# Performance work log

Hardware: AMD Instinct MI355X
Metric: run time of the kernel (lower is better)

## Reference

```python
import jax, jax.numpy as jnp
import numpy as np

LEAKY_SLOPE = 0.2
EPS = 1e-9


def setup_inputs() -> dict:
    key = jax.random.key(0)
    k1, k2, k3, k4 = jax.random.split(key, 4)
    B, N, F_in, F_out = 4, 4096, 128, 64
    h = jax.random.normal(k1, (B, N, F_in), dtype=jnp.float32)
    adj = jax.random.uniform(k2, (B, N, N), dtype=jnp.float32)
    W = jax.random.normal(k3, (F_in, F_out), dtype=jnp.float32) * (1.0 / np.sqrt(F_in))
    a = jax.random.normal(k4, (2 * F_out, 1), dtype=jnp.float32) * (1.0 / np.sqrt(2 * F_out))
    return {"h": h, "adj": adj, "W": W, "a": a}


def reference(h, adj, W, a):
    # h: [B,N,F_in], adj: [B,N,N], W: [F_in,F_out], a: [2F_out,1]
    Wh = jnp.einsum('bnf,fo->bno', h, W)  # [B,N,F_out]
    F_out = W.shape[1]
    a1 = a[:F_out, 0]   # applied to Wh1 (neighbor j features)
    a2 = a[F_out:, 0]   # applied to Wh2 (center i features)
    s1 = Wh @ a1        # [B,N] -> broadcast over j axis
    s2 = Wh @ a2        # [B,N] -> broadcast over i axis
    # e[b,i,j] = leaky_relu(Wh[b,j]@a1 + Wh[b,i]@a2)  (concat([Wh1,Wh2]) @ a)
    e = jax.nn.leaky_relu(s2[:, :, None] + s1[:, None, :], negative_slope=LEAKY_SLOPE)
    attn = jax.nn.softmax(e, axis=-1)          # dense softmax over all nodes
    attn = attn * adj                          # mask with adjacency
    attn = attn / (jnp.sum(attn, axis=-1, keepdims=True) + EPS)  # renormalize
    return jnp.einsum('bij,bjo->bio', attn, Wh)  # [B,N,F_out]
```

## Files before the change

### kernel.cpp

```cpp
#include <hip/hip_runtime.h>
#include <hip/hip_bf16.h>


typedef __attribute__((ext_vector_type(8))) short bf16x8;
typedef __attribute__((ext_vector_type(4))) float f32x4;
typedef __attribute__((ext_vector_type(4))) unsigned int u32x4;

#define LOG2E 1.4426950408889634f

__device__ __forceinline__ unsigned int pk2(float lo, float hi) {
  float2 f2; f2.x = lo; f2.y = hi;
  union { __hip_bfloat162 b; unsigned int u; } c;
  c.b = __float22bfloat162_rn(f2);
  return c.u;
}
__device__ __forceinline__ bf16x8 u2b(u32x4 v) {
  union { u32x4 u; bf16x8 b; } c; c.u = v; return c.b;
}
__device__ __forceinline__ float vexp2_(float x) {
  float r; asm("v_exp_f32 %0, %1" : "=v"(r) : "v"(x)); return r;
}

__global__ __launch_bounds__(256) void k_wh(
    const float* __restrict__ h, const float* __restrict__ W, const float* __restrict__ a,
    unsigned short* __restrict__ wt, float* __restrict__ s1, float* __restrict__ s2) {
  __shared__ float hs[32][130];
  __shared__ float Ws[128 * 64];
  const int t = threadIdx.x;
  const int b = blockIdx.x >> 7;
  const int row0 = (blockIdx.x & 127) << 5;

  #pragma unroll
  for (int it = 0; it < 8; ++it) {
    const int fidx = it * 256 + t;
    ((float4*)Ws)[fidx] = ((const float4*)W)[fidx];
  }
  #pragma unroll
  for (int it = 0; it < 4; ++it) {
    int flat = it * 256 + t;
    int r = flat >> 5, q = flat & 31;
    const float4 v = *(const float4*)(h + ((size_t)(b * 4096 + row0 + r)) * 128 + 4 * q);
    hs[r][4*q+0] = v.x; hs[r][4*q+1] = v.y; hs[r][4*q+2] = v.z; hs[r][4*q+3] = v.w;
  }
  __syncthreads();

  const int rg = t >> 4, cg = t & 15;
  float acc[2][4] = {};
  for (int k = 0; k < 128; ++k) {
    float4 wv = ((const float4*)Ws)[k * 16 + cg];
    #pragma unroll
    for (int i = 0; i < 2; ++i) {
      float hv = hs[2*rg + i][k];
      acc[i][0] = fmaf(hv, wv.x, acc[i][0]);
      acc[i][1] = fmaf(hv, wv.y, acc[i][1]);
      acc[i][2] = fmaf(hv, wv.z, acc[i][2]);
      acc[i][3] = fmaf(hv, wv.w, acc[i][3]);
    }
  }
  __syncthreads();

  float (*WhF)[68] = (float(*)[68])hs;
  #pragma unroll
  for (int i = 0; i < 2; ++i)
    #pragma unroll
    for (int j = 0; j < 4; ++j)
      WhF[2*rg + i][4*cg + j] = acc[i][j];
  __syncthreads();

  if (t < 32) {
    float x1 = 0.f, x2 = 0.f;
    #pragma unroll 8
    for (int c = 0; c < 64; ++c) {
      float v = WhF[t][c];
      x1 = fmaf(v, a[c], x1);
      x2 = fmaf(v, a[64 + c], x2);
    }
    s1[b * 4096 + row0 + t] = x1 * LOG2E;
    s2[b * 4096 + row0 + t] = x2 * LOG2E;
  }

  const int col = t >> 2, sub = t & 3;
  unsigned int uh[4];
  #pragma unroll
  for (int r = 0; r < 4; ++r)
    uh[r] = pk2(WhF[8*sub + 2*r][col], WhF[8*sub + 2*r + 1][col]);
  const int S = (b * 128 + (row0 >> 5)) * 4 + (col >> 4);
  unsigned short* dst = wt + ((size_t)S << 9) + sub * 128 + (col & 15) * 8;
  *(uint4*)dst = make_uint4(uh[0], uh[1], uh[2], uh[3]);
}

__global__ __launch_bounds__(256, 2) void k_main(
    const float* __restrict__ adj, const unsigned short* __restrict__ wt,
    const float* __restrict__ s1, const float* __restrict__ s2,
    float* __restrict__ out) {
  __shared__ unsigned short Pws[2][8192];
  __shared__ float Ss[32];

  const int t = threadIdx.x;
  const int blk = blockIdx.x;
  const int xcd = blk & 7;
  const int b = xcd >> 1;
  const int tile = (blk >> 3) + ((xcd & 1) << 6);
  const int row0 = tile << 5;
  const int l = t & 63, w = t >> 6;
  const int lr = l & 15, g = l >> 4;

  const float* adjW = adj + ((size_t)(b * 4096 + row0 + 8 * w)) * 4096 + 4 * l;
  const float* s1W  = s1 + b * 4096 + 4 * l;
  const unsigned short* wtW = wt + (((size_t)(b * 128) * 4 + w) << 9) + 8 * l;

  float s2r[8];
  #pragma unroll
  for (int r = 0; r < 8; ++r) s2r[r] = s2[b * 4096 + row0 + 8 * w + r];

  float sar[8] = {0.f,0.f,0.f,0.f,0.f,0.f,0.f,0.f};
  f32x4 acc0 = {0.f,0.f,0.f,0.f}, acc1 = {0.f,0.f,0.f,0.f};

  f32x4 aX[8], aY[8], sX, sY;
  u32x4 bv[8];

#define LOADADJ(av, sv, ks) do {                                              \
    const int ko = ((ks) & 15) << 8;                                          \
    _Pragma("unroll")                                                         \
    for (int r = 0; r < 8; ++r)                                               \
      av[r] = *(const f32x4*)(adjW + (size_t)r * 4096 + ko);                  \
    sv = *(const f32x4*)(s1W + ko);                                           \
  } while (0)

#define LOADB(ks) do {                                                        \
    const int ksm = (ks) & 15;                                                \
    const unsigned short* bp = wtW + ((size_t)(ksm * 8) << 11);               \
    _Pragma("unroll")                                                         \
    for (int kk = 0; kk < 8; ++kk)                                            \
      bv[kk] = *(const u32x4*)(bp + (kk << 11));                              \
  } while (0)

#define PBUILD(av, sv, buf) do {                                              \
    unsigned short* Pd = &Pws[buf][0];                                        \
    _Pragma("unroll")                                                         \
    for (int r = 0; r < 8; ++r) {                                             \
      float e0 = s2r[r] + sv[0], e1 = s2r[r] + sv[1];                         \
      float e2 = s2r[r] + sv[2], e3 = s2r[r] + sv[3];                         \
      e0 = fmaxf(e0, 0.2f * e0); e1 = fmaxf(e1, 0.2f * e1);                   \
      e2 = fmaxf(e2, 0.2f * e2); e3 = fmaxf(e3, 0.2f * e3);                   \
      float p0 = vexp2_(e0), p1 = vexp2_(e1);                                 \
      float p2 = vexp2_(e2), p3 = vexp2_(e3);                                 \
      float w0 = av[r][0] * p0, w1 = av[r][1] * p1;                           \
      float w2 = av[r][2] * p2, w3 = av[r][3] * p3;                           \
      sar[r] += (w0 + w1) + (w2 + w3);                                        \
      uint2 pk; pk.x = pk2(w0, w1); pk.y = pk2(w2, w3);                       \
      *(uint2*)(Pd + (8 * w + r) * 256 + ((4 * l) ^ (r << 3))) = pk;          \
    }                                                                         \
  } while (0)

#define SYNC() do {                                                           \
    asm volatile("s_waitcnt lgkmcnt(0)" ::: "memory");                        \
    __builtin_amdgcn_sched_barrier(0);                                        \
    __builtin_amdgcn_s_barrier();                                             \
    __builtin_amdgcn_sched_barrier(0);                                        \
  } while (0)

#define MFMAP(buf) do {                                                       \
    const unsigned short* Pr = &Pws[buf][0];                                  \
    _Pragma("unroll")                                                         \
    for (int kk = 0; kk < 8; ++kk) {                                          \
      const int koff = (8 * g + 32 * kk) ^ ((lr & 7) << 3);                   \
      bf16x8 a0 = *(const bf16x8*)(Pr + lr * 256 + koff);                     \
      bf16x8 a1 = *(const bf16x8*)(Pr + (16 + lr) * 256 + koff);              \
      acc0 = __builtin_amdgcn_mfma_f32_16x16x32_bf16(a0, u2b(bv[kk]), acc0, 0, 0, 0); \
      acc1 = __builtin_amdgcn_mfma_f32_16x16x32_bf16(a1, u2b(bv[kk]), acc1, 0, 0, 0); \
    }                                                                         \
  } while (0)

  LOADADJ(aX, sX, 0);
  LOADADJ(aY, sY, 1);
  LOADB(0);

  for (int it = 0; it < 8; ++it) {
    PBUILD(aX, sX, 0);
    LOADADJ(aX, sX, 2 * it + 2);
    SYNC();
    MFMAP(0);
    LOADB(2 * it + 1);

    PBUILD(aY, sY, 1);
    LOADADJ(aY, sY, 2 * it + 3);
    SYNC();
    MFMAP(1);
    LOADB(2 * it + 2);
  }

  #pragma unroll
  for (int r = 0; r < 8; ++r) {
    float v = sar[r];
    #pragma unroll
    for (int m = 1; m < 64; m <<= 1) v += __shfl_xor(v, m);
    sar[r] = v;
  }
  if (l == 0) {
    #pragma unroll
    for (int r = 0; r < 8; ++r) Ss[8 * w + r] = sar[r];
  }
  __syncthreads();

  #pragma unroll
  for (int reg = 0; reg < 4; ++reg) {
    const int r0 = 4 * g + reg, r1 = 16 + 4 * g + reg;
    const float i0 = 1.0f / Ss[r0], i1 = 1.0f / Ss[r1];
    const size_t ob = ((size_t)(b * 4096 + row0 + r0)) * 64 + 16 * w + lr;
    out[ob] = acc0[reg] * i0;
    out[ob + (size_t)16 * 64] = acc1[reg] * i1;
  }
}

extern "C" void kernel_launch(void* const* d_in, const int* in_sizes, int n_in,
                              void* d_out, int out_size, void* d_ws, size_t ws_size,
                              hipStream_t stream) {
  const float* h   = (const float*)d_in[0];
  const float* adj = (const float*)d_in[1];
  const float* W   = (const float*)d_in[2];
  const float* a   = (const float*)d_in[3];
  float* out = (float*)d_out;

  unsigned short* wt = (unsigned short*)d_ws;
  float* s1 = (float*)(wt + (size_t)4 * 64 * 4096);
  float* s2 = s1 + 16384;

  k_wh  <<<512, 256, 0, stream>>>(h, W, a, wt, s1, s2);
  k_main<<<512, 256, 0, stream>>>(adj, wt, s1, s2, out);
}
```

Baseline: 60.93 us.

## Double the k-chunk per pipeline stage in the attention aggregation kernel

Each pipeline stage now processes 512 neighbor columns instead of 256. Every thread therefore prefetches twice as many adjacency float4 values, and the P tile in LDS grows to 32x512 bf16 per buffer. This halves the number of barrier-synchronized steps and keeps more adjacency loads in flight, aimed at the HBM-bound stream over adj. In exchange, register and LDS use roughly double, and the W·h B-operand loads for the second half are issued just before their MFMAs, which may expose their latency.

```diff
diff --git a/kernel.cpp b/kernel.cpp
--- a/kernel.cpp
+++ b/kernel.cpp
@@ -93,7 +93,7 @@
     const float* __restrict__ adj, const unsigned short* __restrict__ wt,
     const float* __restrict__ s1, const float* __restrict__ s2,
     float* __restrict__ out) {
-  __shared__ unsigned short Pws[2][8192];
+  __shared__ unsigned short Pws[2][32 * 512];
   __shared__ float Ss[32];
 
   const int t = threadIdx.x;
@@ -107,7 +107,7 @@
 
   const float* adjW = adj + ((size_t)(b * 4096 + row0 + 8 * w)) * 4096 + 4 * l;
   const float* s1W  = s1 + b * 4096 + 4 * l;
-  const unsigned short* wtW = wt + (((size_t)(b * 128) * 4 + w) << 9) + 8 * l;
+  const unsigned short* wtW = wt + (((size_t)b * 512 + w) << 9) + 8 * l;
 
   float s2r[8];
   #pragma unroll
@@ -116,40 +116,46 @@
   float sar[8] = {0.f,0.f,0.f,0.f,0.f,0.f,0.f,0.f};
   f32x4 acc0 = {0.f,0.f,0.f,0.f}, acc1 = {0.f,0.f,0.f,0.f};
 
-  f32x4 aX[8], aY[8], sX, sY;
+  f32x4 aX[8][2], aY[8][2], sX[2], sY[2];
   u32x4 bv[8];
 
 #define LOADADJ(av, sv, ks) do {                                              \
-    const int ko = ((ks) & 15) << 8;                                          \
-    _Pragma("unroll")                                                         \
-    for (int r = 0; r < 8; ++r)                                               \
-      av[r] = *(const f32x4*)(adjW + (size_t)r * 4096 + ko);                  \
-    sv = *(const f32x4*)(s1W + ko);                                           \
-  } while (0)
-
-#define LOADB(ks) do {                                                        \
-    const int ksm = (ks) & 15;                                                \
-    const unsigned short* bp = wtW + ((size_t)(ksm * 8) << 11);               \
+    const int ko = ((ks) & 7) << 9;                                           \
+    _Pragma("unroll")                                                         \
+    for (int r = 0; r < 8; ++r) {                                             \
+      av[r][0] = *(const f32x4*)(adjW + (size_t)r * 4096 + ko);               \
+      av[r][1] = *(const f32x4*)(adjW + (size_t)r * 4096 + ko + 256);         \
+    }                                                                         \
+    sv[0] = *(const f32x4*)(s1W + ko);                                        \
+    sv[1] = *(const f32x4*)(s1W + ko + 256);                                  \
+  } while (0)
+
+#define LOADBH(ks, ph) do {                                                   \
     _Pragma("unroll")                                                         \
     for (int kk = 0; kk < 8; ++kk)                                            \
-      bv[kk] = *(const u32x4*)(bp + (kk << 11));                              \
+      bv[kk] = *(const u32x4*)(wtW + (size_t)((ks) * 16 + (ph) * 8 + kk) * 2048); \
   } while (0)
 
 #define PBUILD(av, sv, buf) do {                                              \
     unsigned short* Pd = &Pws[buf][0];                                        \
     _Pragma("unroll")                                                         \
     for (int r = 0; r < 8; ++r) {                                             \
-      float e0 = s2r[r] + sv[0], e1 = s2r[r] + sv[1];                         \
-      float e2 = s2r[r] + sv[2], e3 = s2r[r] + sv[3];                         \
-      e0 = fmaxf(e0, 0.2f * e0); e1 = fmaxf(e1, 0.2f * e1);                   \
-      e2 = fmaxf(e2, 0.2f * e2); e3 = fmaxf(e3, 0.2f * e3);                   \
-      float p0 = vexp2_(e0), p1 = vexp2_(e1);                                 \
-      float p2 = vexp2_(e2), p3 = vexp2_(e3);                                 \
-      float w0 = av[r][0] * p0, w1 = av[r][1] * p1;                           \
-      float w2 = av[r][2] * p2, w3 = av[r][3] * p3;                           \
-      sar[r] += (w0 + w1) + (w2 + w3);                                        \
-      uint2 pk; pk.x = pk2(w0, w1); pk.y = pk2(w2, w3);                       \
-      *(uint2*)(Pd + (8 * w + r) * 256 + ((4 * l) ^ (r << 3))) = pk;          \
+      const int rl = 8 * w + r;                                               \
+      const int sw = (rl & 7) << 3;                                           \
+      _Pragma("unroll")                                                       \
+      for (int hh = 0; hh < 2; ++hh) {                                        \
+        float e0 = s2r[r] + sv[hh][0], e1 = s2r[r] + sv[hh][1];               \
+        float e2 = s2r[r] + sv[hh][2], e3 = s2r[r] + sv[hh][3];               \
+        e0 = fmaxf(e0, 0.2f * e0); e1 = fmaxf(e1, 0.2f * e1);                 \
+        e2 = fmaxf(e2, 0.2f * e2); e3 = fmaxf(e3, 0.2f * e3);                 \
+        float p0 = vexp2_(e0), p1 = vexp2_(e1);                               \
+        float p2 = vexp2_(e2), p3 = vexp2_(e3);                               \
+        float w0 = av[r][hh][0] * p0, w1 = av[r][hh][1] * p1;                 \
+        float w2 = av[r][hh][2] * p2, w3 = av[r][hh][3] * p3;                 \
+        sar[r] += (w0 + w1) + (w2 + w3);                                      \
+        uint2 pk; pk.x = pk2(w0, w1); pk.y = pk2(w2, w3);                     \
+        *(uint2*)(Pd + rl * 512 + ((256 * hh + 4 * l) ^ sw)) = pk;            \
+      }                                                                       \
     }                                                                         \
   } while (0)
 
@@ -160,34 +166,34 @@
     __builtin_amdgcn_sched_barrier(0);                                        \
   } while (0)
 
-#define MFMAP(buf) do {                                                       \
+#define MFMAH(buf, ph) do {                                                   \
     const unsigned short* Pr = &Pws[buf][0];                                  \
     _Pragma("unroll")                                                         \
     for (int kk = 0; kk < 8; ++kk) {                                          \
-      const int koff = (8 * g + 32 * kk) ^ ((lr & 7) << 3);                   \
-      bf16x8 a0 = *(const bf16x8*)(Pr + lr * 256 + koff);                     \
-      bf16x8 a1 = *(const bf16x8*)(Pr + (16 + lr) * 256 + koff);              \
+      const int koff = (8 * g + 32 * ((ph) * 8 + kk)) ^ ((lr & 7) << 3);      \
+      bf16x8 a0 = *(const bf16x8*)(Pr + lr * 512 + koff);                     \
+      bf16x8 a1 = *(const bf16x8*)(Pr + (16 + lr) * 512 + koff);              \
       acc0 = __builtin_amdgcn_mfma_f32_16x16x32_bf16(a0, u2b(bv[kk]), acc0, 0, 0, 0); \
       acc1 = __builtin_amdgcn_mfma_f32_16x16x32_bf16(a1, u2b(bv[kk]), acc1, 0, 0, 0); \
     }                                                                         \
   } while (0)
 
+#define STEP(av, sv, buf, s) do {                                             \
+    LOADBH(s, 0);                      \
+    PBUILD(av, sv, buf);                                                      \
+    LOADADJ(av, sv, (s) + 2);               \
+    SYNC();                          \
+    MFMAH(buf, 0);                                                            \
+    LOADBH(s, 1);                        \
+    MFMAH(buf, 1);                                                            \
+  } while (0)
+
   LOADADJ(aX, sX, 0);
   LOADADJ(aY, sY, 1);
-  LOADB(0);
-
-  for (int it = 0; it < 8; ++it) {
-    PBUILD(aX, sX, 0);
-    LOADADJ(aX, sX, 2 * it + 2);
-    SYNC();
-    MFMAP(0);
-    LOADB(2 * it + 1);
-
-    PBUILD(aY, sY, 1);
-    LOADADJ(aY, sY, 2 * it + 3);
-    SYNC();
-    MFMAP(1);
-    LOADB(2 * it + 2);
+
+  for (int it = 0; it < 4; ++it) {
+    STEP(aX, sX, 0, 2 * it);
+    STEP(aY, sY, 1, 2 * it + 1);
   }
 
   #pragma unroll
```

Result: slower. 199.9 us (+228.1%).
